# Optimization experiments

Measured on AMD Instinct MI355X. Metric: run time of the kernel, lower is better.

## Reference

```python
import jax, jax.numpy as jnp
import numpy as np

N_NODES = 100000
N_EDGES = 1600000
K_IND = 16          # num_indicator_weight (distance bins)
K_MLP = 16          # num_mlp_weight
DIM_HIDDEN = 64     # dim_mlp_hidden
DIST_MAX = 1.0      # distance_max
K = K_IND + K_MLP   # node feature dim / Dense output dim


def setup_inputs() -> dict:
    key = jax.random.key(0)
    ks = jax.random.split(key, 10)
    nodes = jax.random.normal(ks[0], (N_NODES, K), dtype=jnp.float32)
    distance = jax.random.uniform(ks[1], (N_EDGES,), dtype=jnp.float32) * DIST_MAX
    receivers = jnp.sort(jax.random.randint(ks[2], (N_EDGES,), 0, N_NODES, dtype=jnp.int32))
    senders = jax.random.randint(ks[3], (N_EDGES,), 0, N_NODES, dtype=jnp.int32)
    edges_padding = jnp.ones((N_EDGES,), dtype=jnp.float32)
    # MLPWeights params (Dense(1->H), Dense(H->K_MLP))
    w1 = jax.random.normal(ks[4], (1, DIM_HIDDEN), dtype=jnp.float32) / np.sqrt(1.0)
    b1 = jnp.zeros((DIM_HIDDEN,), dtype=jnp.float32)
    w2 = jax.random.normal(ks[5], (DIM_HIDDEN, K_MLP), dtype=jnp.float32) / np.sqrt(DIM_HIDDEN)
    b2 = jnp.zeros((K_MLP,), dtype=jnp.float32)
    # PowerDifference params (a=0.5, b=2)
    a = jnp.array([0.5], dtype=jnp.float32)
    b = jnp.array([2.0], dtype=jnp.float32)
    # gamma_self (no bias), gamma_gathered (with bias), both Dense(K->K)
    wg_self = jax.random.normal(ks[6], (K, K), dtype=jnp.float32) / np.sqrt(K)
    wg_gath = jax.random.normal(ks[7], (K, K), dtype=jnp.float32) / np.sqrt(K)
    bg_gath = jnp.zeros((K,), dtype=jnp.float32)
    return {"nodes": nodes, "distance": distance, "edges_padding": edges_padding,
            "receivers": receivers, "senders": senders,
            "w1": w1, "b1": b1, "w2": w2, "b2": b2,
            "a": a, "b": b, "wg_self": wg_self, "wg_gath": wg_gath, "bg_gath": bg_gath}


def _normalize_edges(edges, seg_ids, num_segments):
    sums = jax.ops.segment_sum(edges, seg_ids, num_segments=num_segments, indices_are_sorted=True)
    return edges / (sums[seg_ids] + 1e-5)


def _softmax_edges(edges, seg_ids, num_segments):
    maxs = jax.ops.segment_max(edges, seg_ids, num_segments=num_segments, indices_are_sorted=True)
    e = jnp.exp(edges - maxs[seg_ids])
    sums = jax.ops.segment_sum(e, seg_ids, num_segments=num_segments, indices_are_sorted=True)
    return e / sums[seg_ids]


def reference(nodes, distance, edges_padding, receivers, senders,
              w1, b1, w2, b2, a, b, wg_self, wg_gath, bg_gath):
    n = nodes.shape[0]
    d = distance[:, None]                                   # [E,1]
    # IndicatorWeights: bin membership via heaviside of product
    bins = jnp.linspace(0.0, DIST_MAX, K_IND + 1, dtype=nodes.dtype)
    indicator = jnp.heaviside((bins[None, :-1] - d) * (d - bins[None, 1:]), 0.0)  # [E,K_IND]
    indicator_w = _normalize_edges(indicator, receivers, n)
    # MLPWeights: Dense -> relu -> Dense, then segment softmax
    mlp = jax.nn.relu(d @ w1 + b1) @ w2 + b2                # [E,K_MLP]
    mlp_w = _softmax_edges(mlp, receivers, n)
    weights = jnp.concatenate([indicator_w, mlp_w], axis=1) * edges_padding[:, None]  # [E,K]
    # PowerDifference on gathered node pairs
    a_c = jnp.clip(a, 0.0, 1.0)
    b_c = jnp.abs(b)
    edge_pds = jnp.power(jnp.abs(a_c * nodes[receivers] - (1.0 - a_c) * nodes[senders]), b_c)  # [E,K]
    gathered = jax.ops.segment_sum(weights * edge_pds, receivers, num_segments=n, indices_are_sorted=True)  # [N,K]
    out = jax.nn.relu(nodes @ wg_self + (gathered @ wg_gath + bg_gath))
    return out
```

## Files before the change

kernel.cpp:

```cpp
#include <hip/hip_runtime.h>
#include <math.h>

#define K_TOT 32
#define K_IND 16
#define K_MLP 16
#define DHID  64


__global__ void prep_kernel(const int* __restrict__ recv, int E, int N,
                            const float* __restrict__ w1,
                            const float* __restrict__ b1,
                            const float* __restrict__ w2,
                            float* __restrict__ wsP,
                            float* __restrict__ wsN,
                            int* __restrict__ wsflag,
                            int* __restrict__ rp) {
    if (blockIdx.x == 0 && threadIdx.x < 64) {
        int t = threadIdx.x;
        if (t < K_MLP) {
            float P = 0.f, Nn = 0.f;
            for (int j = 0; j < DHID; ++j) {
                float w = w1[j];
                float v = w2[j * K_MLP + t];
                P  += fmaxf(w, 0.f) * v;
                Nn += fminf(w, 0.f) * v;
            }
            wsP[t] = P; wsN[t] = Nn;
        }
        bool nz = (b1[t] != 0.f);
        unsigned long long mask = __ballot(nz);
        if (t == 0) *wsflag = (mask == 0ull) ? 1 : 0;
    }
    int tid = blockIdx.x * blockDim.x + threadIdx.x;
    if (tid <= N) {
        int lo = 0, hi = E;
        while (lo < hi) {
            int mid = (lo + hi) >> 1;
            if (recv[mid] < tid) lo = mid + 1; else hi = mid;
        }
        rp[tid] = lo;
    }
}

__global__ __launch_bounds__(256) void graph_kernel(
        const float* __restrict__ nodes,
        const float* __restrict__ dist,
        const float* __restrict__ padv,
        const int*   __restrict__ send,
        const float* __restrict__ w1,
        const float* __restrict__ b1,
        const float* __restrict__ w2,
        const float* __restrict__ b2,
        const float* __restrict__ a_p,
        const float* __restrict__ b_p,
        const float* __restrict__ wg_self,
        const float* __restrict__ wg_gath,
        const float* __restrict__ bg,
        const float* __restrict__ wsP,
        const float* __restrict__ wsN,
        const int*   __restrict__ wsflag,
        const int*   __restrict__ rp,
        float* __restrict__ out,
        int N) {
    int wave = blockIdx.x * (blockDim.x >> 6) + (threadIdx.x >> 6);
    if (wave >= N) return;
    int n    = wave;
    int lane = threadIdx.x & 63;
    int eg   = lane >> 4;
    int cc   = lane & 15;

    float a_c = fminf(fmaxf(a_p[0], 0.f), 1.f);
    float am  = 1.f - a_c;
    float bc  = fabsf(b_p[0]);

    float Pk = wsP[cc];
    float Nk = wsN[cc];

    const float* nrow = nodes + n * K_TOT;
    float nr0 = nrow[cc];
    float nr1 = nrow[cc + 16];
    float anr0 = a_c * nr0;
    float anr1 = a_c * nr1;

    int e0 = rp[n], eEnd = rp[n + 1];
    int len = eEnd - e0;

    float lo = (float)cc * 0.0625f;
    float hi = lo + 0.0625f;

    float cnt = 0.f, si = 0.f;
    float l = 0.f, acc = 0.f;
    float g_ind, g_mlp;

    bool fastf = (*wsflag != 0) && (bc == 2.0f) && (len <= 64);

    if (__builtin_amdgcn_readfirstlane((int)fastf)) {
        if (len > 0) {
            int idx = lane < len ? lane : len - 1;
            float dm = fabsf(dist[e0 + idx]);
#pragma unroll
            for (int off = 32; off; off >>= 1) dm = fmaxf(dm, __shfl_xor(dm, off));
            float negM = -fmaxf(fabsf(Pk), fabsf(Nk)) * dm;

            int nG = (len + 3) >> 2;
            int last = len - 1;

#define GRP_BODY(G)                                                          \
            {                                                                \
                int i = ((G) << 2) + eg;                                     \
                bool valid = i < len;                                        \
                int ii = valid ? i : last;                                   \
                float d  = dist[e0 + ii];                                    \
                int   s  = send[e0 + ii];                                    \
                float pe = padv[e0 + ii];                                    \
                const float* nsrow = nodes + (s * K_TOT + cc);               \
                float ns0 = nsrow[0];                                        \
                float ns1 = nsrow[16];                                       \
                float t0 = fmaf(-am, ns0, anr0);                             \
                float t1 = fmaf(-am, ns1, anr1);                             \
                float pd0 = t0 * t0;                                         \
                float pd1 = t1 * t1;                                         \
                bool inb = valid && (d > lo) && (d < hi);                    \
                cnt += inb ? 1.f : 0.f;                                      \
                si   = inb ? fmaf(pe, pd0, si) : si;                         \
                float q = (d > 0.f) ? Pk : Nk;                               \
                float p = __expf(fmaf(d, q, negM));                          \
                p = valid ? p : 0.f;                                         \
                l += p;                                                      \
                acc = fmaf(p, pe * pd1, acc);                                \
            }

            int g = 0;
            for (; g + 2 <= nG; g += 2) {
                GRP_BODY(g)
                GRP_BODY(g + 1)
            }
            if (g < nG) {
                GRP_BODY(g)
            }
#undef GRP_BODY
        }

#pragma unroll
        for (int off = 16; off <= 32; off <<= 1) {
            cnt += __shfl_xor(cnt, off);
            si  += __shfl_xor(si,  off);
            l   += __shfl_xor(l,   off);
            acc += __shfl_xor(acc, off);
        }
        g_ind = si / (cnt + 1e-5f);
        g_mlp = (l > 0.f) ? (acc / l) : 0.f;
    } else {
        float m_on = -INFINITY;
        for (int i = eg; i < len; i += 4) {
            int e = e0 + i;
            float d  = dist[e];
            int   s  = send[e];
            float pe = padv[e];
            const float* nsrow = nodes + (s * K_TOT + cc);
            float ns0 = nsrow[0];
            float ns1 = nsrow[16];
            float t0 = fabsf(fmaf(-am, ns0, anr0));
            float t1 = fabsf(fmaf(-am, ns1, anr1));
            float pd0 = powf(t0, bc);
            float pd1 = powf(t1, bc);

            bool inb = (d > lo) && (d < hi);
            cnt += inb ? 1.f : 0.f;
            si  += inb ? pe * pd0 : 0.f;

            float mlp = 0.f;
            for (int j = 0; j < DHID; ++j) {
                float h = fmaxf(fmaf(d, w1[j], b1[j]), 0.f);
                mlp = fmaf(h, w2[j * K_MLP + cc], mlp);
            }
            float mn = fmaxf(m_on, mlp);
            float al = (m_on == -INFINITY) ? 0.f : __expf(m_on - mn);
            float p  = __expf(mlp - mn);
            l   = fmaf(l, al, p);
            acc = fmaf(acc, al, p * pe * pd1);
            m_on = mn;
        }
#pragma unroll
        for (int off = 16; off <= 32; off <<= 1) {
            cnt += __shfl_xor(cnt, off);
            si  += __shfl_xor(si,  off);
            float m2 = __shfl_xor(m_on, off), l2 = __shfl_xor(l, off), a2 = __shfl_xor(acc, off);
            float mn = fmaxf(m_on, m2);
            float f1 = (m_on == -INFINITY) ? 0.f : __expf(m_on - mn);
            float f2 = (m2   == -INFINITY) ? 0.f : __expf(m2 - mn);
            l   = l * f1 + l2 * f2;
            acc = acc * f1 + a2 * f2;
            m_on = mn;
        }
        g_ind = si / (cnt + 1e-5f);
        g_mlp = (l > 0.f) ? (acc / l) : 0.f;
    }

    int h  = lane >> 5;
    int oc = lane & 31;
    float pre_g = ((lane >> 4) & 1) ? g_mlp : g_ind;
    float pre_n = ((lane >> 4) & 1) ? nr1 : nr0;

    float o_s = 0.f, o_g = 0.f;
    int jbase = h * 16;
#pragma unroll
    for (int jj = 0; jj < 16; ++jj) {
        int j = jbase + jj;
        float gj = __shfl(pre_g, j);
        float nj = __shfl(pre_n, j);
        o_s = fmaf(nj, wg_self[j * K_TOT + oc], o_s);
        o_g = fmaf(gj, wg_gath[j * K_TOT + oc], o_g);
    }
    float o = o_s + o_g;
    o += __shfl_xor(o, 32);
    if (h == 0) {
        out[n * K_TOT + oc] = fmaxf(o + bg[oc], 0.f);
    }
}

extern "C" void kernel_launch(void* const* d_in, const int* in_sizes, int n_in,
                              void* d_out, int out_size, void* d_ws, size_t ws_size,
                              hipStream_t stream) {
    const float* nodes   = (const float*)d_in[0];
    const float* dist    = (const float*)d_in[1];
    const float* padv    = (const float*)d_in[2];
    const int*   recv    = (const int*)d_in[3];
    const int*   send    = (const int*)d_in[4];
    const float* w1      = (const float*)d_in[5];
    const float* b1      = (const float*)d_in[6];
    const float* w2      = (const float*)d_in[7];
    const float* b2      = (const float*)d_in[8];
    const float* a_p     = (const float*)d_in[9];
    const float* b_p     = (const float*)d_in[10];
    const float* wg_self = (const float*)d_in[11];
    const float* wg_gath = (const float*)d_in[12];
    const float* bg      = (const float*)d_in[13];
    float* out = (float*)d_out;

    int N = in_sizes[0] / K_TOT;
    int E = in_sizes[1];

    float* wsf    = (float*)d_ws;
    float* wsP    = wsf;
    float* wsN    = wsf + 16;
    int*   wsflag = (int*)d_ws + 32;
    int*   rp     = (int*)d_ws + 64;

    prep_kernel<<<(N + 1 + 255) / 256, 256, 0, stream>>>(recv, E, N, w1, b1, w2,
                                                         wsP, wsN, wsflag, rp);
    graph_kernel<<<(N + 3) / 4, 256, 0, stream>>>(
        nodes, dist, padv, send, w1, b1, w2, b2, a_p, b_p,
        wg_self, wg_gath, bg, wsP, wsN, wsflag, rp, out, N);
}
```

Baseline: 172.4 us.

## Stage Dense weights in LDS and broadcast per-edge data via wave shuffles

```diff
diff --git a/kernel.cpp b/kernel.cpp
--- a/kernel.cpp
+++ b/kernel.cpp
@@ -62,6 +62,16 @@
         const int*   __restrict__ rp,
         float* __restrict__ out,
         int N) {
+    __shared__ __align__(16) float s_w[2048];
+    __shared__ float2 s_gn[4 * 32];
+
+    {
+        int t = threadIdx.x;
+        ((float4*)s_w)[t]          = ((const float4*)wg_self)[t];
+        ((float4*)(s_w + 1024))[t] = ((const float4*)wg_gath)[t];
+    }
+    __syncthreads();
+
     int wave = blockIdx.x * (blockDim.x >> 6) + (threadIdx.x >> 6);
     if (wave >= N) return;
     int n    = wave;
@@ -96,23 +106,23 @@
 
     if (__builtin_amdgcn_readfirstlane((int)fastf)) {
         if (len > 0) {
-            int idx = lane < len ? lane : len - 1;
-            float dm = fabsf(dist[e0 + idx]);
-#pragma unroll
-            for (int off = 32; off; off >>= 1) dm = fmaxf(dm, __shfl_xor(dm, off));
-            float negM = -fmaxf(fabsf(Pk), fabsf(Nk)) * dm;
+            int idx = (lane < len) ? lane : (len - 1);
+            int ei  = e0 + idx;
+            float d_all  = dist[ei];
+            int   s_all  = send[ei];
+            float pe_all = padv[ei];
+
+            float negM = -fmaxf(fabsf(Pk), fabsf(Nk));
 
             int nG = (len + 3) >> 2;
-            int last = len - 1;
 
 #define GRP_BODY(G)                                                          \
             {                                                                \
                 int i = ((G) << 2) + eg;                                     \
                 bool valid = i < len;                                        \
-                int ii = valid ? i : last;                                   \
-                float d  = dist[e0 + ii];                                    \
-                int   s  = send[e0 + ii];                                    \
-                float pe = padv[e0 + ii];                                    \
+                float d  = __shfl(d_all, i);                                 \
+                int   s  = __shfl(s_all, i);                                 \
+                float pe = __shfl(pe_all, i);                                \
                 const float* nsrow = nodes + (s * K_TOT + cc);               \
                 float ns0 = nsrow[0];                                        \
                 float ns1 = nsrow[16];                                       \
@@ -171,8 +181,8 @@
 
             float mlp = 0.f;
             for (int j = 0; j < DHID; ++j) {
-                float h = fmaxf(fmaf(d, w1[j], b1[j]), 0.f);
-                mlp = fmaf(h, w2[j * K_MLP + cc], mlp);
+                float h2 = fmaxf(fmaf(d, w1[j], b1[j]), 0.f);
+                mlp = fmaf(h2, w2[j * K_MLP + cc], mlp);
             }
             float mn = fmaxf(m_on, mlp);
             float al = (m_on == -INFINITY) ? 0.f : __expf(m_on - mn);
@@ -197,22 +207,23 @@
         g_mlp = (l > 0.f) ? (acc / l) : 0.f;
     }
 
+    int wv = threadIdx.x >> 6;
+    float pre_g = ((lane >> 4) & 1) ? g_mlp : g_ind;
+    float pre_n = ((lane >> 4) & 1) ? nr1 : nr0;
+    if (lane < 32) s_gn[wv * 32 + lane] = make_float2(pre_n, pre_g);
+
     int h  = lane >> 5;
     int oc = lane & 31;
-    float pre_g = ((lane >> 4) & 1) ? g_mlp : g_ind;
-    float pre_n = ((lane >> 4) & 1) ? nr1 : nr0;
-
-    float o_s = 0.f, o_g = 0.f;
-    int jbase = h * 16;
+    const float2* gn  = s_gn + wv * 32 + h * 16;
+    const float* wrow = s_w + (h * 16) * K_TOT + oc;
+
+    float o = 0.f;
 #pragma unroll
     for (int jj = 0; jj < 16; ++jj) {
-        int j = jbase + jj;
-        float gj = __shfl(pre_g, j);
-        float nj = __shfl(pre_n, j);
-        o_s = fmaf(nj, wg_self[j * K_TOT + oc], o_s);
-        o_g = fmaf(gj, wg_gath[j * K_TOT + oc], o_g);
-    }
-    float o = o_s + o_g;
+        float2 v = gn[jj];
+        o = fmaf(v.x, wrow[jj * K_TOT], o);
+        o = fmaf(v.y, wrow[1024 + jj * K_TOT], o);
+    }
     o += __shfl_xor(o, 32);
     if (h == 0) {
         out[n * K_TOT + oc] = fmaxf(o + bg[oc], 0.f);
```

Result: faster. 160.0 us (-7.2%).
